# Kernel tuning notes

Hardware: AMD Instinct MI355X
Metric: run time of the kernel (lower is better)

The kernel has to match this reference:

```python
import jax, jax.numpy as jnp
import numpy as np

KH, KW = 5, 5  # kernel_size
B, C, H, W = 4, 3, 1024, 1024


def setup_inputs() -> dict:
    key = jax.random.key(0)
    x = jax.random.normal(key, (B, C, H, W), dtype=jnp.float32)
    return {"input": x}


def _median_blur(x, kh, kw):
    # zero padding identical to _compute_zero_padding: (k-1)//2 per side -> 'same' output
    ph, pw = (kh - 1) // 2, (kw - 1) // 2
    b, c, h, w = x.shape
    xp = jnp.pad(x, ((0, 0), (0, 0), (ph, ph), (pw, pw)))
    # Materialize the kh*kw shifted views (same math as conv2d with binary kernel / im2col)
    patches = jnp.stack(
        [xp[:, :, i:i + h, j:j + w] for i in range(kh) for j in range(kw)],
        axis=2,
    )  # [B, C, kh*kw, H, W]
    # torch.median(dim=2)[0]: for odd kh*kw this is the exact middle order statistic
    sorted_p = jnp.sort(patches, axis=2)
    mid = (kh * kw - 1) // 2
    return sorted_p[:, :, mid, :, :]


def reference(input) -> jnp.ndarray:
    return _median_blur(input, KH, KW)
```

## Files before the change

### kernel.cpp

```cpp
#include <hip/hip_runtime.h>

#define CAS(a, b) { float _t = fminf(a, b); (b) = fmaxf(a, b); (a) = _t; }
#define MED3(a,b,c) __builtin_amdgcn_fmed3f((a),(b),(c))

#define IMG    1024
#define TW     128
#define TH     8
#define RAW_W  136
#define RAW_H  12

__device__ __forceinline__ void sort5(float& a0, float& a1, float& a2, float& a3, float& a4) {
    CAS(a0, a1); CAS(a3, a4); CAS(a2, a4); CAS(a2, a3);
    CAS(a0, a3); CAS(a0, a2); CAS(a1, a4); CAS(a1, a3); CAS(a1, a2);
}

__device__ __forceinline__ float tail13v(const float* cd) {
    float e0 = cd[0],  e1 = cd[1];
    float f0 = cd[2],  f1 = cd[3],  f2 = cd[4];
    float h0 = cd[5],  h1 = cd[6],  h2 = cd[7];
    float g0 = cd[8],  g1 = cd[9],  g2 = cd[10];
    float k0 = cd[11], k1 = cd[12];

    float A0 = fminf(e0, f0), M = fmaxf(e0, f0);
    float A4 = f2;
    float A3 = fmaxf(e1, f1);
    float A1 = fminf(fminf(M, e1), f1);
    float A2 = MED3(e1, f1, M);
    float C0 = g0;
    float C4 = fmaxf(g2, k1);
    float C1 = fminf(g1, k0);
    float mgk = fminf(g2, k1);
    float C3 = fmaxf(fmaxf(mgk, g1), k0);
    float C2 = MED3(g1, k0, mgk);
    float r3 = fmaxf(fmaxf(fmaxf(fminf(A0, C3), fminf(A1, C2)), fminf(A2, C1)), fminf(A3, C0));
    float r4 = fmaxf(fmaxf(fmaxf(fminf(A0, C4), fminf(A1, C3)), fminf(A2, C2)),
                     fmaxf(fminf(A3, C1), fminf(A4, C0)));
    float r5 = fmaxf(fmaxf(fmaxf(fminf(A1, C4), fminf(A2, C3)), fminf(A3, C2)),
                     fmaxf(fmaxf(fminf(A4, C1), A0), C0));
    float r6 = fmaxf(fmaxf(fmaxf(fminf(A2, C4), fminf(A3, C3)), fminf(A4, C2)),
                     fmaxf(A1, C1));
    return fmaxf(fmaxf(fmaxf(fminf(r4, h2), fminf(r5, h1)), fminf(r6, h0)), r3);
}

__global__ __launch_bounds__(256, 4)
void median5x5_kernel(const float* __restrict__ in, float* __restrict__ out) {
    __shared__ float tile[RAW_H][RAW_W];
    __shared__ float scol[5][TH][RAW_W];

    const int tx  = threadIdx.x;
    const int ty  = threadIdx.y;
    const int tid = ty * 32 + tx;
    const int x0  = blockIdx.x * TW;
    const int y0  = blockIdx.y * TH;
    const float* plane = in + (size_t)blockIdx.z * (IMG * IMG);

    #pragma unroll
    for (int t = tid; t < RAW_H * (RAW_W / 4); t += 256) {
        int r   = t / 34;
        int k   = t - r * 34;
        int gy  = y0 - 2 + r;
        int gx0 = x0 - 4 + 4 * k;
        float4 v = make_float4(0.f, 0.f, 0.f, 0.f);
        if ((unsigned)gy < IMG && (unsigned)gx0 < IMG)
            v = *(const float4*)(plane + (size_t)gy * IMG + gx0);
        *(float4*)&tile[r][4 * k] = v;
    }
    __syncthreads();

    for (int p = tx; p < 66; p += 32) {
        int c = 2 * p + 2;
        float2 r0 = *(const float2*)&tile[ty + 0][c];
        float2 r1 = *(const float2*)&tile[ty + 1][c];
        float2 r2 = *(const float2*)&tile[ty + 2][c];
        float2 r3 = *(const float2*)&tile[ty + 3][c];
        float2 r4 = *(const float2*)&tile[ty + 4][c];
        sort5(r0.x, r1.x, r2.x, r3.x, r4.x);
        sort5(r0.y, r1.y, r2.y, r3.y, r4.y);
        *(float2*)&scol[0][ty][c] = r0;
        *(float2*)&scol[1][ty][c] = r1;
        *(float2*)&scol[2][ty][c] = r2;
        *(float2*)&scol[3][ty][c] = r3;
        *(float2*)&scol[4][ty][c] = r4;
    }
    __syncthreads();

    const int cb = 4 * tx + 2;
    float cd[4][13];

    #pragma unroll
    for (int i = 0; i < 5; ++i) {
        const float* rp = &scol[i][ty][cb];
        float2 u0 = *(const float2*)(rp);
        float2 u1 = *(const float2*)(rp + 2);
        float2 u2 = *(const float2*)(rp + 4);
        float2 u3 = *(const float2*)(rp + 6);
        float c0 = u0.x, c1 = u0.y, c2 = u1.x, c3 = u1.y;
        float c4 = u2.x, c5 = u2.y, c6 = u3.x, c7 = u3.y;

        float m0 = c3, m1 = c4; CAS(m0, m1);
        float a = c1, b = c2; CAS(a, b);
        float s0 = fminf(a, m0), t1 = fmaxf(a, m0);
        float t2 = fminf(b, m1), s3 = fmaxf(b, m1);
        float s1 = fminf(t1, t2), s2 = fmaxf(t1, t2);
        float d = c5, e = c6; CAS(d, e);
        float q0 = fminf(m0, d), w1 = fmaxf(m0, d);
        float w2 = fminf(m1, e), q3 = fmaxf(m1, e);
        float q1 = fminf(w1, w2), q2 = fmaxf(w1, w2);

#define EXT(px, S0, S1, S2, S3, X) { \
        if (i == 0)      { cd[px][0]  = MED3(S2, S3, X); cd[px][1]  = fmaxf(S3, X); } \
        else if (i == 1) { cd[px][2]  = MED3(S1, S2, X); cd[px][3]  = MED3(S2, S3, X); cd[px][4] = fmaxf(S3, X); } \
        else if (i == 2) { cd[px][5]  = MED3(S0, S1, X); cd[px][6]  = MED3(S1, S2, X); cd[px][7] = MED3(S2, S3, X); } \
        else if (i == 3) { cd[px][8]  = fminf(S0, X);    cd[px][9]  = MED3(S0, S1, X); cd[px][10] = MED3(S1, S2, X); } \
        else             { cd[px][11] = fminf(S0, X);    cd[px][12] = MED3(S0, S1, X); } }
        EXT(0, s0, s1, s2, s3, c0)
        EXT(1, s0, s1, s2, s3, c5)
        EXT(2, q0, q1, q2, q3, c2)
        EXT(3, q0, q1, q2, q3, c7)
#undef EXT
    }

    float4 o;
    o.x = tail13v(cd[0]);
    o.y = tail13v(cd[1]);
    o.z = tail13v(cd[2]);
    o.w = tail13v(cd[3]);
    *(float4*)(out + (size_t)blockIdx.z * (IMG * IMG) + (size_t)(y0 + ty) * IMG + x0 + 4 * tx) = o;
}

extern "C" void kernel_launch(void* const* d_in, const int* in_sizes, int n_in,
                              void* d_out, int out_size, void* d_ws, size_t ws_size,
                              hipStream_t stream) {
    const float* in  = (const float*)d_in[0];
    float*       out = (float*)d_out;
    dim3 block(32, TH, 1);
    dim3 grid(IMG / TW, IMG / TH, 12);
    hipLaunchKernelGGL(median5x5_kernel, grid, block, 0, stream, in, out);
}
```

Baseline: 135.1 us.

## Load column sort inputs directly from global memory and swizzle shared columns

Result: no change. 137.0 us (+1.4%).

```diff
diff --git a/kernel.cpp b/kernel.cpp
--- a/kernel.cpp
+++ b/kernel.cpp
@@ -7,7 +7,8 @@
 #define TW     128
 #define TH     8
 #define RAW_W  136
-#define RAW_H  12
+
+#define SWZ(P) ((P) ^ ((((P) >> 4) & 1) << 3) ^ ((((P) >> 5) & 1) << 2))
 
 __device__ __forceinline__ void sort5(float& a0, float& a1, float& a2, float& a3, float& a4) {
     CAS(a0, a1); CAS(a3, a4); CAS(a2, a4); CAS(a2, a3);
@@ -42,58 +43,59 @@
     return fmaxf(fmaxf(fmaxf(fminf(r4, h2), fminf(r5, h1)), fminf(r6, h0)), r3);
 }
 
-__global__ __launch_bounds__(256, 4)
+__global__ __launch_bounds__(256, 6)
 void median5x5_kernel(const float* __restrict__ in, float* __restrict__ out) {
-    __shared__ float tile[RAW_H][RAW_W];
     __shared__ float scol[5][TH][RAW_W];
 
     const int tx  = threadIdx.x;
     const int ty  = threadIdx.y;
-    const int tid = ty * 32 + tx;
     const int x0  = blockIdx.x * TW;
     const int y0  = blockIdx.y * TH;
     const float* plane = in + (size_t)blockIdx.z * (IMG * IMG);
+    const int gy0 = y0 + ty - 2;
 
-    #pragma unroll
-    for (int t = tid; t < RAW_H * (RAW_W / 4); t += 256) {
-        int r   = t / 34;
-        int k   = t - r * 34;
-        int gy  = y0 - 2 + r;
-        int gx0 = x0 - 4 + 4 * k;
-        float4 v = make_float4(0.f, 0.f, 0.f, 0.f);
-        if ((unsigned)gy < IMG && (unsigned)gx0 < IMG)
-            v = *(const float4*)(plane + (size_t)gy * IMG + gx0);
-        *(float4*)&tile[r][4 * k] = v;
-    }
+    auto ldp = [&](int gy, int gxb) -> float2 {
+        float2 v = make_float2(0.f, 0.f);
+        if ((unsigned)gy < IMG && (unsigned)gxb < IMG)
+            v = *(const float2*)(plane + (size_t)gy * IMG + gxb);
+        return v;
+    };
+
+#define TASK(p) { \
+        int gxb = x0 - 2 + 2 * (p); \
+        float2 r0 = ldp(gy0 + 0, gxb); \
+        float2 r1 = ldp(gy0 + 1, gxb); \
+        float2 r2 = ldp(gy0 + 2, gxb); \
+        float2 r3 = ldp(gy0 + 3, gxb); \
+        float2 r4 = ldp(gy0 + 4, gxb); \
+        sort5(r0.x, r1.x, r2.x, r3.x, r4.x); \
+        sort5(r0.y, r1.y, r2.y, r3.y, r4.y); \
+        int cs = 2 * SWZ((p) + 1); \
+        *(float2*)&scol[0][ty][cs] = r0; \
+        *(float2*)&scol[1][ty][cs] = r1; \
+        *(float2*)&scol[2][ty][cs] = r2; \
+        *(float2*)&scol[3][ty][cs] = r3; \
+        *(float2*)&scol[4][ty][cs] = r4; }
+    TASK(tx);
+    TASK(tx + 32);
+    if (tx < 2) TASK(tx + 64);
+#undef TASK
     __syncthreads();
 
-    for (int p = tx; p < 66; p += 32) {
-        int c = 2 * p + 2;
-        float2 r0 = *(const float2*)&tile[ty + 0][c];
-        float2 r1 = *(const float2*)&tile[ty + 1][c];
-        float2 r2 = *(const float2*)&tile[ty + 2][c];
-        float2 r3 = *(const float2*)&tile[ty + 3][c];
-        float2 r4 = *(const float2*)&tile[ty + 4][c];
-        sort5(r0.x, r1.x, r2.x, r3.x, r4.x);
-        sort5(r0.y, r1.y, r2.y, r3.y, r4.y);
-        *(float2*)&scol[0][ty][c] = r0;
-        *(float2*)&scol[1][ty][c] = r1;
-        *(float2*)&scol[2][ty][c] = r2;
-        *(float2*)&scol[3][ty][c] = r3;
-        *(float2*)&scol[4][ty][c] = r4;
-    }
-    __syncthreads();
-
-    const int cb = 4 * tx + 2;
+    const int P0 = 2 * tx + 1;
+    const int o0 = 2 * SWZ(P0 + 0);
+    const int o1 = 2 * SWZ(P0 + 1);
+    const int o2 = 2 * SWZ(P0 + 2);
+    const int o3 = 2 * SWZ(P0 + 3);
     float cd[4][13];
 
     #pragma unroll
     for (int i = 0; i < 5; ++i) {
-        const float* rp = &scol[i][ty][cb];
-        float2 u0 = *(const float2*)(rp);
-        float2 u1 = *(const float2*)(rp + 2);
-        float2 u2 = *(const float2*)(rp + 4);
-        float2 u3 = *(const float2*)(rp + 6);
+        const float* rp = &scol[i][ty][0];
+        float2 u0 = *(const float2*)(rp + o0);
+        float2 u1 = *(const float2*)(rp + o1);
+        float2 u2 = *(const float2*)(rp + o2);
+        float2 u3 = *(const float2*)(rp + o3);
         float c0 = u0.x, c1 = u0.y, c2 = u1.x, c3 = u1.y;
         float c4 = u2.x, c5 = u2.y, c6 = u3.x, c7 = u3.y;
 
```
